# Kernel tuning notes

Hardware: AMD Instinct MI355X
Metric: run time of the kernel (lower is better)

The kernel has to match this reference:

```python
import jax, jax.numpy as jnp
import numpy as np
from jax import lax

T, B, S = 64, 64, 64
H, E, V, L = 1024, 1024, 50000, 2
PAD = 0


def setup_inputs() -> dict:
    key = jax.random.key(0)
    ks = jax.random.split(key, 12)
    sc_e = 1.0 / np.sqrt(E)
    sc_h = 1.0 / np.sqrt(H)
    inp = {
        "input": jax.random.randint(ks[0], (T, B), 0, V),
        "h0": jax.random.normal(ks[1], (L, B, H), jnp.float32),
        "c0": jax.random.normal(ks[2], (L, B, H), jnp.float32),
        "context": jax.random.normal(ks[3], (S, B, H), jnp.float32),
        # embedding table, padding row zeroed (padding_idx)
        "emb": (jax.random.normal(ks[4], (V, E), jnp.float32) * sc_e).at[PAD].set(0.0),
        # stacked LSTM params, torch gate order i,f,g,o (E == H so layers stack)
        "w_ih": jax.random.uniform(ks[5], (L, 4 * H, H), jnp.float32, -sc_h, sc_h),
        "w_hh": jax.random.uniform(ks[6], (L, 4 * H, H), jnp.float32, -sc_h, sc_h),
        "b_ih": jax.random.uniform(ks[7], (L, 4 * H), jnp.float32, -sc_h, sc_h),
        "b_hh": jax.random.uniform(ks[8], (L, 4 * H), jnp.float32, -sc_h, sc_h),
        # GlobalAttention: linear_in (H->H, no bias), linear_out (2H->H, no bias)
        "w_in": jax.random.uniform(ks[9], (H, H), jnp.float32, -sc_h, sc_h),
        "w_out": jax.random.uniform(ks[10], (H, 2 * H), jnp.float32, -sc_h, sc_h),
    }
    return inp


def _decode(input, h0, c0, context, emb, w_ih, w_hh, b_ih, b_hh, w_in, w_out):
    ctx = jnp.transpose(context, (1, 0, 2))  # [B, S, H] (context.t())
    x = emb[input]                           # [T, B, E]
    n_layers = w_ih.shape[0]

    def step(carry, x_t):
        h, c = carry  # each [L, B, H]
        layer_in = x_t
        hs, cs = [], []
        for l in range(n_layers):
            gates = layer_in @ w_ih[l].T + h[l] @ w_hh[l].T + b_ih[l] + b_hh[l]
            i, f, g, o = jnp.split(gates, 4, axis=-1)
            c_l = jax.nn.sigmoid(f) * c[l] + jax.nn.sigmoid(i) * jnp.tanh(g)
            h_l = jax.nn.sigmoid(o) * jnp.tanh(c_l)
            hs.append(h_l)
            cs.append(c_l)
            layer_in = h_l
        h_new, c_new = jnp.stack(hs), jnp.stack(cs)
        # GlobalAttention (Luong general)
        q = layer_in @ w_in.T                          # [B, H]
        scores = jnp.einsum("bsh,bh->bs", ctx, q)       # [B, S]
        a = jax.nn.softmax(scores, axis=-1)
        wc = jnp.einsum("bs,bsh->bh", a, ctx)           # [B, H]
        out = jnp.tanh(jnp.concatenate([wc, layer_in], axis=-1) @ w_out.T)
        return (h_new, c_new), (out, a)

    (h_f, c_f), (outs, attns) = lax.scan(step, (h0, c0), x)
    return outs, h_f, c_f, attns[-1]


def reference(input, h0, c0, context, emb, w_ih, w_hh, b_ih, b_hh, w_in, w_out):
    return _decode(input, h0, c0, context, emb, w_ih, w_hh, b_ih, b_hh, w_in, w_out)
```

## Files before the change

kernel.cpp:

```cpp
#include <hip/hip_runtime.h>

typedef _Float16 f16;
typedef __attribute__((ext_vector_type(4))) _Float16 f16x4;
typedef __attribute__((ext_vector_type(8))) _Float16 f16x8;
typedef __attribute__((ext_vector_type(4))) float f32x4;

__device__ __forceinline__ float fast_sig(float x) { return 1.f / (1.f + __expf(-x)); }
__device__ __forceinline__ float fast_tanh(float x) {
  float e = __expf(2.f * x);
  return 1.f - 2.f / (e + 1.f);
}

__global__ __launch_bounds__(256) void f2h_kernel(const float* __restrict__ src,
                                                  f16* __restrict__ dst) {
  size_t i = ((size_t)blockIdx.x * 256 + threadIdx.x) * 4;
  float4 v = *(const float4*)(src + i);
  dst[i + 0] = (f16)v.x;
  dst[i + 1] = (f16)v.y;
  dst[i + 2] = (f16)v.z;
  dst[i + 3] = (f16)v.w;
}

__global__ __launch_bounds__(256) void gather_rows(const float* __restrict__ emb,
                                                   const int* __restrict__ ids,
                                                   f16* __restrict__ xg) {
  int m = blockIdx.x;
  int i = threadIdx.x * 4;
  const float* src = emb + (size_t)ids[m] * 1024 + i;
  float4 v = *(const float4*)src;
  f16* d = xg + (size_t)m * 1024 + i;
  d[0] = (f16)v.x; d[1] = (f16)v.y; d[2] = (f16)v.z; d[3] = (f16)v.w;
}

__global__ __launch_bounds__(256) void init_h(const float* __restrict__ h0,
                                              f16* __restrict__ h1slot0,
                                              f16* __restrict__ h2slot0,
                                              unsigned* __restrict__ flags) {
  int i = blockIdx.x * 256 + threadIdx.x;
  h1slot0[i] = (f16)h0[i];
  h2slot0[i] = (f16)h0[65536 + i];
  if (i < 8192) flags[i] = 0;
}

__global__ __launch_bounds__(512, 1) void lstm_persistent(
    const float* __restrict__ w_ih, const float* __restrict__ w_hh,
    const float* __restrict__ b_ih, const float* __restrict__ b_hh,
    const float* __restrict__ c0,
    const f16* __restrict__ xg,
    f16* __restrict__ h1hist,
    f16* __restrict__ h2hist,
    float* __restrict__ hf, float* __restrict__ cf,
    unsigned* __restrict__ flags) {
  __shared__ f16 wlds[65536];
  __shared__ float red1[2048], red2[2048];
  __shared__ float bsum[32];
  const int p = blockIdx.x;
  const int tid = threadIdx.x;
  const int lane = tid & 63, w = tid >> 6;
  const int mt = w & 3, kh = w >> 2;
  const int am = mt * 16 + (lane & 15);
  const int kq = (lane >> 4) * 8;

  for (int s = tid; s < 8192; s += 512) {
    const int mat = s >> 11, sl = s & 2047;
    const int ln = sl & 63, ks = sl >> 6;
    const int n = ln & 15;
    const int row = (n >> 2) * 1024 + p * 4 + (n & 3) + ((mat >= 2) ? 4096 : 0);
    const int k = ks * 32 + (ln >> 4) * 8;
    const float* src = ((mat & 1) ? w_hh : w_ih) + (size_t)row * 1024 + k;
    float4 v0 = *(const float4*)src;
    float4 v1 = *(const float4*)(src + 4);
    f16x8 hv = {(f16)v0.x, (f16)v0.y, (f16)v0.z, (f16)v0.w,
                (f16)v1.x, (f16)v1.y, (f16)v1.z, (f16)v1.w};
    *(f16x8*)(wlds + (size_t)mat * 16384 + (size_t)sl * 8) = hv;
  }
  if (tid < 32) {
    int l = tid >> 4, n = tid & 15;
    int row = l * 4096 + (n >> 2) * 1024 + p * 4 + (n & 3);
    bsum[tid] = b_ih[row] + b_hh[row];
  }
  float creg;
  {
    int q = tid & 255;
    size_t idx = (size_t)(q >> 2) * 1024 + p * 4 + (q & 3);
    creg = (tid < 256) ? c0[idx] : c0[65536 + idx];
  }
  __syncthreads();

  for (int t = 0; t <= 64; ++t) {
    const int tx = (t < 64) ? t : 63;
    const int t2 = (t > 0) ? t - 1 : 0;
    const f16* xrow  = xg + ((size_t)tx * 64 + am) * 1024 + kh * 512 + kq;
    const f16* hrow  = h1hist + ((size_t)t * 64 + am) * 1024 + kh * 512 + kq;
    const f16* h2row = h2hist + ((size_t)t2 * 64 + am) * 1024 + kh * 512 + kq;

    f32x4 acc1 = {0.f, 0.f, 0.f, 0.f};
    f32x4 acc2 = {0.f, 0.f, 0.f, 0.f};
#pragma unroll
    for (int i = 0; i < 16; ++i) {
      const int ks = kh * 16 + i;
      f16x8 xv  = *(const f16x8*)(xrow + i * 32);
      f16x8 hv  = *(const f16x8*)(hrow + i * 32);
      f16x8 h2v = *(const f16x8*)(h2row + i * 32);
      f16x8 b0 = *(const f16x8*)(wlds + (size_t)ks * 512 + lane * 8);
      f16x8 b1 = *(const f16x8*)(wlds + 16384 + (size_t)ks * 512 + lane * 8);
      f16x8 b2 = *(const f16x8*)(wlds + 32768 + (size_t)ks * 512 + lane * 8);
      f16x8 b3 = *(const f16x8*)(wlds + 49152 + (size_t)ks * 512 + lane * 8);
      if (t < 64) {
        acc1 = __builtin_amdgcn_mfma_f32_16x16x32_f16(xv, b0, acc1, 0, 0, 0);
        acc1 = __builtin_amdgcn_mfma_f32_16x16x32_f16(hv, b1, acc1, 0, 0, 0);
      }
      if (t > 0) {
        acc2 = __builtin_amdgcn_mfma_f32_16x16x32_f16(hv, b2, acc2, 0, 0, 0);
        acc2 = __builtin_amdgcn_mfma_f32_16x16x32_f16(h2v, b3, acc2, 0, 0, 0);
      }
    }

    if (t < 64) {
#pragma unroll
      for (int q = 0; q < 4; q++)
        red1[w * 256 + ((lane >> 4) * 4 + q) * 16 + (lane & 15)] = acc1[q];
    }
    if (t > 0) {
#pragma unroll
      for (int q = 0; q < 4; q++)
        red2[w * 256 + ((lane >> 4) * 4 + q) * 16 + (lane & 15)] = acc2[q];
    }
    __syncthreads();

    if (t < 64 && tid < 256) {
      const int b = tid >> 2, ul = tid & 3;
      const int mrow = (b & 15) * 16, mtb = (b >> 4) * 256;
      float g4[4];
#pragma unroll
      for (int g = 0; g < 4; g++) {
        int n = g * 4 + ul;
        g4[g] = red1[mtb + mrow + n] + red1[1024 + mtb + mrow + n] + bsum[n];
      }
      float cn = fast_sig(g4[1]) * creg + fast_sig(g4[0]) * fast_tanh(g4[2]);
      float hn = fast_sig(g4[3]) * fast_tanh(cn);
      creg = cn;
      const int u = p * 4 + ul;
      if (t == 63) {
        hf[(size_t)b * 1024 + u] = hn;
        cf[(size_t)b * 1024 + u] = cn;
      }
      float h1v = __shfl_down(hn, 1, 64);
      float h2s = __shfl_down(hn, 2, 64);
      float h3v = __shfl_down(hn, 3, 64);
      if (ul == 0) {
        union { f16x4 h; unsigned long long u64; } pk;
        pk.h = (f16x4){(f16)hn, (f16)h1v, (f16)h2s, (f16)h3v};
        f16* dst = h1hist + (size_t)(t + 1) * 65536 + (size_t)b * 1024 + p * 4;
        __hip_atomic_store((unsigned long long*)dst, pk.u64,
                           __ATOMIC_RELAXED, __HIP_MEMORY_SCOPE_AGENT);
      }
    }
    if (t > 0 && tid >= 256) {
      const int q = tid & 255;
      const int b = q >> 2, ul = q & 3;
      const int mrow = (b & 15) * 16, mtb = (b >> 4) * 256;
      float g4[4];
#pragma unroll
      for (int g = 0; g < 4; g++) {
        int n = g * 4 + ul;
        g4[g] = red2[mtb + mrow + n] + red2[1024 + mtb + mrow + n] + bsum[16 + n];
      }
      float cn = fast_sig(g4[1]) * creg + fast_sig(g4[0]) * fast_tanh(g4[2]);
      float hn = fast_sig(g4[3]) * fast_tanh(cn);
      creg = cn;
      const int u = p * 4 + ul;
      if (t == 64) {
        hf[65536 + (size_t)b * 1024 + u] = hn;
        cf[65536 + (size_t)b * 1024 + u] = cn;
      }
      float h1v = __shfl_down(hn, 1, 64);
      float h2s = __shfl_down(hn, 2, 64);
      float h3v = __shfl_down(hn, 3, 64);
      if (ul == 0) {
        union { f16x4 h; unsigned long long u64; } pk;
        pk.h = (f16x4){(f16)hn, (f16)h1v, (f16)h2s, (f16)h3v};
        f16* dst = h2hist + (size_t)t * 65536 + (size_t)b * 1024 + p * 4;
        __hip_atomic_store((unsigned long long*)dst, pk.u64,
                           __ATOMIC_RELAXED, __HIP_MEMORY_SCOPE_AGENT);
      }
    }

    if (t < 64) {
      __syncthreads();
      const unsigned epoch = (unsigned)(t + 1);
      if (w == 0) {
        if (lane == 0)
          __hip_atomic_store(flags + (size_t)p * 16, epoch,
                             __ATOMIC_RELAXED, __HIP_MEMORY_SCOPE_AGENT);
        if (p == 0) {
          for (;;) {
            bool ok = true;
#pragma unroll
            for (int j = 0; j < 4; j++) {
              unsigned v = __hip_atomic_load(flags + (size_t)(lane * 4 + j) * 16,
                                             __ATOMIC_RELAXED, __HIP_MEMORY_SCOPE_AGENT);
              ok &= (v >= epoch);
            }
            if (__all(ok)) break;
            __builtin_amdgcn_s_sleep(1);
          }
          if (lane < 8)
            __hip_atomic_store(flags + 4096 + (size_t)lane * 16, epoch,
                               __ATOMIC_RELAXED, __HIP_MEMORY_SCOPE_AGENT);
        } else {
          const unsigned* go = flags + 4096 + (size_t)(p & 7) * 16;
          for (;;) {
            unsigned v = __hip_atomic_load(go, __ATOMIC_RELAXED,
                                           __HIP_MEMORY_SCOPE_AGENT);
            if (__all(v >= epoch)) break;
            __builtin_amdgcn_s_sleep(1);
          }
        }
      }
      __syncthreads();
    }
  }
}

template <typename OutT>
__global__ __launch_bounds__(256) void gemm_simple(
    const f16* __restrict__ A1, const f16* __restrict__ A2,
    const f16* __restrict__ Bm,
    const float* __restrict__ bias1, const float* __restrict__ bias2,
    OutT* __restrict__ C, int ldc,
    int K1, int Ktot, int do_tanh) {
  const int tid = threadIdx.x;
  const int lane = tid & 63;
  const int w = tid >> 6;
  const int m0 = blockIdx.y * 64 + w * 16;
  const int n0 = blockIdx.x * 64;
  const int am = m0 + (lane & 15);
  const int kq = (lane >> 4) * 8;
  const int K2 = Ktot - K1;

  f32x4 acc[4];
#pragma unroll
  for (int j = 0; j < 4; j++) acc[j] = (f32x4){0.f, 0.f, 0.f, 0.f};

  for (int k0 = 0; k0 < Ktot; k0 += 32) {
    int k = k0 + kq;
    f16x8 av;
    if (k < K1)
      av = *(const f16x8*)(A1 + (size_t)am * K1 + k);
    else
      av = *(const f16x8*)(A2 + (size_t)am * K2 + (k - K1));
#pragma unroll
    for (int j = 0; j < 4; j++) {
      f16x8 bv = *(const f16x8*)(Bm + (size_t)(n0 + j * 16 + (lane & 15)) * Ktot + k);
      acc[j] = __builtin_amdgcn_mfma_f32_16x16x32_f16(av, bv, acc[j], 0, 0, 0);
    }
  }

  const int r0 = (lane >> 4) * 4;
  const int cc = lane & 15;
#pragma unroll
  for (int j = 0; j < 4; j++) {
    int col = n0 + j * 16 + cc;
    float bv = 0.f;
    if (bias1) bv += bias1[col];
    if (bias2) bv += bias2[col];
#pragma unroll
    for (int q = 0; q < 4; q++) {
      float v = acc[j][q] + bv;
      if (do_tanh) v = fast_tanh(v);
      C[(size_t)(m0 + r0 + q) * ldc + col] = (OutT)v;
    }
  }
}

__global__ __launch_bounds__(256) void attn_kernel(
    const float* __restrict__ Q,
    const float* __restrict__ ctx,
    f16* __restrict__ wc,
    float* __restrict__ attn_out) {
  const int m = blockIdx.x;
  const int b = m & 63;
  const int t = m >> 6;
  const int tid = threadIdx.x;
  const int lane = tid & 63;
  const int w = tid >> 6;
  __shared__ float s_sc[64];
  __shared__ float s_at[64];

  const float* qp = Q + (size_t)m * 1024 + lane * 16;
  float qf[16];
#pragma unroll
  for (int i = 0; i < 4; i++) {
    float4 v = *(const float4*)(qp + i * 4);
    qf[i * 4 + 0] = v.x; qf[i * 4 + 1] = v.y; qf[i * 4 + 2] = v.z; qf[i * 4 + 3] = v.w;
  }

  for (int si = 0; si < 16; si++) {
    int s = w * 16 + si;
    const float* cp = ctx + ((size_t)s * 64 + b) * 1024 + lane * 16;
    float d = 0.f;
#pragma unroll
    for (int i = 0; i < 4; i++) {
      float4 v = *(const float4*)(cp + i * 4);
      d += v.x * qf[i * 4] + v.y * qf[i * 4 + 1] + v.z * qf[i * 4 + 2] + v.w * qf[i * 4 + 3];
    }
#pragma unroll
    for (int off = 32; off > 0; off >>= 1) d += __shfl_down(d, off, 64);
    if (lane == 0) s_sc[s] = d;
  }
  __syncthreads();
  if (w == 0) {
    float v = s_sc[lane];
    float mx = v;
#pragma unroll
    for (int off = 32; off > 0; off >>= 1) mx = fmaxf(mx, __shfl_xor(mx, off, 64));
    float e = __expf(v - mx);
    float sm = e;
#pragma unroll
    for (int off = 32; off > 0; off >>= 1) sm += __shfl_xor(sm, off, 64);
    float a = e / sm;
    s_at[lane] = a;
    if (t == 63) attn_out[b * 64 + lane] = a;
  }
  __syncthreads();
#pragma unroll
  for (int rep = 0; rep < 4; rep++) {
    int h = rep * 256 + tid;
    float acc = 0.f;
    for (int s = 0; s < 64; s++)
      acc += s_at[s] * ctx[((size_t)s * 64 + b) * 1024 + h];
    wc[(size_t)m * 1024 + h] = (f16)acc;
  }
}

extern "C" void kernel_launch(void* const* d_in, const int* in_sizes, int n_in,
                              void* d_out, int out_size, void* d_ws, size_t ws_size,
                              hipStream_t stream) {
  const int*   input = (const int*)d_in[0];
  const float* h0    = (const float*)d_in[1];
  const float* c0    = (const float*)d_in[2];
  const float* ctx   = (const float*)d_in[3];
  const float* emb   = (const float*)d_in[4];
  const float* w_ih  = (const float*)d_in[5];
  const float* w_hh  = (const float*)d_in[6];
  const float* b_ih  = (const float*)d_in[7];
  const float* b_hh  = (const float*)d_in[8];
  const float* w_in  = (const float*)d_in[9];
  const float* w_out = (const float*)d_in[10];
  float* out = (float*)d_out;

  char* ws = (char*)d_ws;
  size_t off = 0;
  auto alloc = [&](size_t bytes) {
    char* p = ws + off;
    off += (bytes + 255) & ~(size_t)255;
    return p;
  };
  f16*   h2hist = (f16*)alloc((size_t)65 * 65536 * 2);
  f16*   h1hist = (f16*)alloc((size_t)65 * 65536 * 2);
  float* Q      = (float*)alloc((size_t)4096 * 1024 * 4);
  f16*   wc     = (f16*)alloc((size_t)4096 * 1024 * 2);
  f16*   xg     = (f16*)alloc((size_t)4096 * 1024 * 2);
  f16*   winh   = (f16*)alloc((size_t)1024 * 1024 * 2);
  f16*   wouth  = (f16*)alloc((size_t)1024 * 2048 * 2);
  unsigned* flags = (unsigned*)alloc(32768);

  float* outs = out;
  float* hf   = out + (size_t)4096 * 1024;
  float* cf   = hf + 131072;
  float* attn = cf + 131072;

  f2h_kernel<<<1024, 256, 0, stream>>>(w_in, winh);
  f2h_kernel<<<2048, 256, 0, stream>>>(w_out, wouth);
  gather_rows<<<4096, 256, 0, stream>>>(emb, input, xg);
  init_h<<<256, 256, 0, stream>>>(h0, h1hist, h2hist, flags);

  {
    void* args[] = {(void*)&w_ih, (void*)&w_hh, (void*)&b_ih, (void*)&b_hh,
                    (void*)&c0, (void*)&xg, (void*)&h1hist, (void*)&h2hist,
                    (void*)&hf, (void*)&cf, (void*)&flags};
    hipLaunchCooperativeKernel(lstm_persistent, dim3(256), dim3(512), args, 0, stream);
  }

  gemm_simple<float><<<dim3(16, 64), 256, 0, stream>>>(h2hist + 65536, nullptr,
      winh, nullptr, nullptr, Q, 1024, 1024, 1024, 0);

  attn_kernel<<<4096, 256, 0, stream>>>(Q, ctx, wc, attn);

  gemm_simple<float><<<dim3(16, 64), 256, 0, stream>>>(wc, h2hist + 65536,
      wouth, nullptr, nullptr, outs, 1024, 1024, 2048, 1);
}
```

Baseline: 1.541 ms.

## Overlap input projection with grid barrier wait and stage GEMM B tiles in LDS

The persistent LSTM loop now issues the x·W_ih MFMAs for the next step before waiting on the grid-wide barrier. The flag arrival store moves to the end of each step, so the input-projection work, which needs no recurrent state, hides barrier latency. Separately, the post-LSTM GEMMs stage 64x64 B tiles in shared memory with register prefetch instead of having each wave read B directly from global memory. This adds a barrier-ordering change that must still protect the h history reads, plus extra syncthreads in the GEMM.

```diff
diff --git a/kernel.cpp b/kernel.cpp
--- a/kernel.cpp
+++ b/kernel.cpp
@@ -96,103 +96,20 @@
 
     f32x4 acc1 = {0.f, 0.f, 0.f, 0.f};
     f32x4 acc2 = {0.f, 0.f, 0.f, 0.f};
-#pragma unroll
-    for (int i = 0; i < 16; ++i) {
-      const int ks = kh * 16 + i;
-      f16x8 xv  = *(const f16x8*)(xrow + i * 32);
-      f16x8 hv  = *(const f16x8*)(hrow + i * 32);
-      f16x8 h2v = *(const f16x8*)(h2row + i * 32);
-      f16x8 b0 = *(const f16x8*)(wlds + (size_t)ks * 512 + lane * 8);
-      f16x8 b1 = *(const f16x8*)(wlds + 16384 + (size_t)ks * 512 + lane * 8);
-      f16x8 b2 = *(const f16x8*)(wlds + 32768 + (size_t)ks * 512 + lane * 8);
-      f16x8 b3 = *(const f16x8*)(wlds + 49152 + (size_t)ks * 512 + lane * 8);
-      if (t < 64) {
+
+    if (t < 64) {
+#pragma unroll
+      for (int i = 0; i < 16; ++i) {
+        const int ks = kh * 16 + i;
+        f16x8 xv = *(const f16x8*)(xrow + i * 32);
+        f16x8 b0 = *(const f16x8*)(wlds + (size_t)ks * 512 + lane * 8);
         acc1 = __builtin_amdgcn_mfma_f32_16x16x32_f16(xv, b0, acc1, 0, 0, 0);
-        acc1 = __builtin_amdgcn_mfma_f32_16x16x32_f16(hv, b1, acc1, 0, 0, 0);
-      }
-      if (t > 0) {
-        acc2 = __builtin_amdgcn_mfma_f32_16x16x32_f16(hv, b2, acc2, 0, 0, 0);
-        acc2 = __builtin_amdgcn_mfma_f32_16x16x32_f16(h2v, b3, acc2, 0, 0, 0);
-      }
-    }
-
-    if (t < 64) {
-#pragma unroll
-      for (int q = 0; q < 4; q++)
-        red1[w * 256 + ((lane >> 4) * 4 + q) * 16 + (lane & 15)] = acc1[q];
-    }
+      }
+    }
+
     if (t > 0) {
-#pragma unroll
-      for (int q = 0; q < 4; q++)
-        red2[w * 256 + ((lane >> 4) * 4 + q) * 16 + (lane & 15)] = acc2[q];
-    }
-    __syncthreads();
-
-    if (t < 64 && tid < 256) {
-      const int b = tid >> 2, ul = tid & 3;
-      const int mrow = (b & 15) * 16, mtb = (b >> 4) * 256;
-      float g4[4];
-#pragma unroll
-      for (int g = 0; g < 4; g++) {
-        int n = g * 4 + ul;
-        g4[g] = red1[mtb + mrow + n] + red1[1024 + mtb + mrow + n] + bsum[n];
-      }
-      float cn = fast_sig(g4[1]) * creg + fast_sig(g4[0]) * fast_tanh(g4[2]);
-      float hn = fast_sig(g4[3]) * fast_tanh(cn);
-      creg = cn;
-      const int u = p * 4 + ul;
-      if (t == 63) {
-        hf[(size_t)b * 1024 + u] = hn;
-        cf[(size_t)b * 1024 + u] = cn;
-      }
-      float h1v = __shfl_down(hn, 1, 64);
-      float h2s = __shfl_down(hn, 2, 64);
-      float h3v = __shfl_down(hn, 3, 64);
-      if (ul == 0) {
-        union { f16x4 h; unsigned long long u64; } pk;
-        pk.h = (f16x4){(f16)hn, (f16)h1v, (f16)h2s, (f16)h3v};
-        f16* dst = h1hist + (size_t)(t + 1) * 65536 + (size_t)b * 1024 + p * 4;
-        __hip_atomic_store((unsigned long long*)dst, pk.u64,
-                           __ATOMIC_RELAXED, __HIP_MEMORY_SCOPE_AGENT);
-      }
-    }
-    if (t > 0 && tid >= 256) {
-      const int q = tid & 255;
-      const int b = q >> 2, ul = q & 3;
-      const int mrow = (b & 15) * 16, mtb = (b >> 4) * 256;
-      float g4[4];
-#pragma unroll
-      for (int g = 0; g < 4; g++) {
-        int n = g * 4 + ul;
-        g4[g] = red2[mtb + mrow + n] + red2[1024 + mtb + mrow + n] + bsum[16 + n];
-      }
-      float cn = fast_sig(g4[1]) * creg + fast_sig(g4[0]) * fast_tanh(g4[2]);
-      float hn = fast_sig(g4[3]) * fast_tanh(cn);
-      creg = cn;
-      const int u = p * 4 + ul;
-      if (t == 64) {
-        hf[65536 + (size_t)b * 1024 + u] = hn;
-        cf[65536 + (size_t)b * 1024 + u] = cn;
-      }
-      float h1v = __shfl_down(hn, 1, 64);
-      float h2s = __shfl_down(hn, 2, 64);
-      float h3v = __shfl_down(hn, 3, 64);
-      if (ul == 0) {
-        union { f16x4 h; unsigned long long u64; } pk;
-        pk.h = (f16x4){(f16)hn, (f16)h1v, (f16)h2s, (f16)h3v};
-        f16* dst = h2hist + (size_t)t * 65536 + (size_t)b * 1024 + p * 4;
-        __hip_atomic_store((unsigned long long*)dst, pk.u64,
-                           __ATOMIC_RELAXED, __HIP_MEMORY_SCOPE_AGENT);
-      }
-    }
-
-    if (t < 64) {
-      __syncthreads();
-      const unsigned epoch = (unsigned)(t + 1);
+      const unsigned epoch = (unsigned)t;
       if (w == 0) {
-        if (lane == 0)
-          __hip_atomic_store(flags + (size_t)p * 16, epoch,
-                             __ATOMIC_RELAXED, __HIP_MEMORY_SCOPE_AGENT);
         if (p == 0) {
           for (;;) {
             bool ok = true;
@@ -220,16 +137,110 @@
       }
       __syncthreads();
     }
+
+#pragma unroll
+    for (int i = 0; i < 16; ++i) {
+      const int ks = kh * 16 + i;
+      f16x8 hv  = *(const f16x8*)(hrow + i * 32);
+      f16x8 h2v = *(const f16x8*)(h2row + i * 32);
+      f16x8 b1 = *(const f16x8*)(wlds + 16384 + (size_t)ks * 512 + lane * 8);
+      f16x8 b2 = *(const f16x8*)(wlds + 32768 + (size_t)ks * 512 + lane * 8);
+      f16x8 b3 = *(const f16x8*)(wlds + 49152 + (size_t)ks * 512 + lane * 8);
+      if (t < 64)
+        acc1 = __builtin_amdgcn_mfma_f32_16x16x32_f16(hv, b1, acc1, 0, 0, 0);
+      if (t > 0) {
+        acc2 = __builtin_amdgcn_mfma_f32_16x16x32_f16(hv, b2, acc2, 0, 0, 0);
+        acc2 = __builtin_amdgcn_mfma_f32_16x16x32_f16(h2v, b3, acc2, 0, 0, 0);
+      }
+    }
+
+    if (t < 64) {
+#pragma unroll
+      for (int q = 0; q < 4; q++)
+        red1[w * 256 + ((lane >> 4) * 4 + q) * 16 + (lane & 15)] = acc1[q];
+    }
+    if (t > 0) {
+#pragma unroll
+      for (int q = 0; q < 4; q++)
+        red2[w * 256 + ((lane >> 4) * 4 + q) * 16 + (lane & 15)] = acc2[q];
+    }
+    __syncthreads();
+
+    if (t < 64 && tid < 256) {
+      const int b = tid >> 2, ul = tid & 3;
+      const int mrow = (b & 15) * 16, mtb = (b >> 4) * 256;
+      float g4[4];
+#pragma unroll
+      for (int g = 0; g < 4; g++) {
+        int n = g * 4 + ul;
+        g4[g] = red1[mtb + mrow + n] + red1[1024 + mtb + mrow + n] + bsum[n];
+      }
+      float cn = fast_sig(g4[1]) * creg + fast_sig(g4[0]) * fast_tanh(g4[2]);
+      float hn = fast_sig(g4[3]) * fast_tanh(cn);
+      creg = cn;
+      const int u = p * 4 + ul;
+      if (t == 63) {
+        hf[(size_t)b * 1024 + u] = hn;
+        cf[(size_t)b * 1024 + u] = cn;
+      }
+      float h1v = __shfl_down(hn, 1, 64);
+      float h2s = __shfl_down(hn, 2, 64);
+      float h3v = __shfl_down(hn, 3, 64);
+      if (ul == 0) {
+        union { f16x4 h; unsigned long long u64; } pk;
+        pk.h = (f16x4){(f16)hn, (f16)h1v, (f16)h2s, (f16)h3v};
+        f16* dst = h1hist + (size_t)(t + 1) * 65536 + (size_t)b * 1024 + p * 4;
+        __hip_atomic_store((unsigned long long*)dst, pk.u64,
+                           __ATOMIC_RELAXED, __HIP_MEMORY_SCOPE_AGENT);
+      }
+    }
+    if (t > 0 && tid >= 256) {
+      const int q = tid & 255;
+      const int b = q >> 2, ul = q & 3;
+      const int mrow = (b & 15) * 16, mtb = (b >> 4) * 256;
+      float g4[4];
+#pragma unroll
+      for (int g = 0; g < 4; g++) {
+        int n = g * 4 + ul;
+        g4[g] = red2[mtb + mrow + n] + red2[1024 + mtb + mrow + n] + bsum[16 + n];
+      }
+      float cn = fast_sig(g4[1]) * creg + fast_sig(g4[0]) * fast_tanh(g4[2]);
+      float hn = fast_sig(g4[3]) * fast_tanh(cn);
+      creg = cn;
+      const int u = p * 4 + ul;
+      if (t == 64) {
+        hf[65536 + (size_t)b * 1024 + u] = hn;
+        cf[65536 + (size_t)b * 1024 + u] = cn;
+      }
+      float h1v = __shfl_down(hn, 1, 64);
+      float h2s = __shfl_down(hn, 2, 64);
+      float h3v = __shfl_down(hn, 3, 64);
+      if (ul == 0) {
+        union { f16x4 h; unsigned long long u64; } pk;
+        pk.h = (f16x4){(f16)hn, (f16)h1v, (f16)h2s, (f16)h3v};
+        f16* dst = h2hist + (size_t)t * 65536 + (size_t)b * 1024 + p * 4;
+        __hip_atomic_store((unsigned long long*)dst, pk.u64,
+                           __ATOMIC_RELAXED, __HIP_MEMORY_SCOPE_AGENT);
+      }
+    }
+
+    if (t < 64) {
+      __syncthreads();
+      if (w == 0 && lane == 0)
+        __hip_atomic_store(flags + (size_t)p * 16, (unsigned)(t + 1),
+                           __ATOMIC_RELAXED, __HIP_MEMORY_SCOPE_AGENT);
+    }
   }
 }
 
 template <typename OutT>
-__global__ __launch_bounds__(256) void gemm_simple(
+__global__ __launch_bounds__(256) void gemm_lds(
     const f16* __restrict__ A1, const f16* __restrict__ A2,
     const f16* __restrict__ Bm,
     const float* __restrict__ bias1, const float* __restrict__ bias2,
     OutT* __restrict__ C, int ldc,
     int K1, int Ktot, int do_tanh) {
+  __shared__ f16 bt[64][72];
   const int tid = threadIdx.x;
   const int lane = tid & 63;
   const int w = tid >> 6;
@@ -238,22 +249,39 @@
   const int am = m0 + (lane & 15);
   const int kq = (lane >> 4) * 8;
   const int K2 = Ktot - K1;
+  const int br = tid >> 2;
+  const int bs = (tid & 3) * 16;
 
   f32x4 acc[4];
 #pragma unroll
   for (int j = 0; j < 4; j++) acc[j] = (f32x4){0.f, 0.f, 0.f, 0.f};
 
-  for (int k0 = 0; k0 < Ktot; k0 += 32) {
-    int k = k0 + kq;
-    f16x8 av;
-    if (k < K1)
-      av = *(const f16x8*)(A1 + (size_t)am * K1 + k);
-    else
-      av = *(const f16x8*)(A2 + (size_t)am * K2 + (k - K1));
-#pragma unroll
-    for (int j = 0; j < 4; j++) {
-      f16x8 bv = *(const f16x8*)(Bm + (size_t)(n0 + j * 16 + (lane & 15)) * Ktot + k);
-      acc[j] = __builtin_amdgcn_mfma_f32_16x16x32_f16(av, bv, acc[j], 0, 0, 0);
+  const f16* bsrc = Bm + (size_t)(n0 + br) * Ktot + bs;
+  f16x8 s0 = *(const f16x8*)(bsrc);
+  f16x8 s1 = *(const f16x8*)(bsrc + 8);
+
+  for (int kc = 0; kc < Ktot; kc += 64) {
+    __syncthreads();
+    *(f16x8*)&bt[br][bs] = s0;
+    *(f16x8*)&bt[br][bs + 8] = s1;
+    __syncthreads();
+    if (kc + 64 < Ktot) {
+      s0 = *(const f16x8*)(bsrc + kc + 64);
+      s1 = *(const f16x8*)(bsrc + kc + 64 + 8);
+    }
+#pragma unroll
+    for (int kk = 0; kk < 64; kk += 32) {
+      int k = kc + kk + kq;
+      f16x8 av;
+      if (k < K1)
+        av = *(const f16x8*)(A1 + (size_t)am * K1 + k);
+      else
+        av = *(const f16x8*)(A2 + (size_t)am * K2 + (k - K1));
+#pragma unroll
+      for (int j = 0; j < 4; j++) {
+        f16x8 bv = *(const f16x8*)&bt[j * 16 + (lane & 15)][kk + kq];
+        acc[j] = __builtin_amdgcn_mfma_f32_16x16x32_f16(av, bv, acc[j], 0, 0, 0);
+      }
     }
   }
 
@@ -383,11 +411,11 @@
     hipLaunchCooperativeKernel(lstm_persistent, dim3(256), dim3(512), args, 0, stream);
   }
 
-  gemm_simple<float><<<dim3(16, 64), 256, 0, stream>>>(h2hist + 65536, nullptr,
+  gemm_lds<float><<<dim3(16, 64), 256, 0, stream>>>(h2hist + 65536, nullptr,
       winh, nullptr, nullptr, Q, 1024, 1024, 1024, 0);
 
   attn_kernel<<<4096, 256, 0, stream>>>(Q, ctx, wc, attn);
 
-  gemm_simple<float><<<dim3(16, 64), 256, 0, stream>>>(wc, h2hist + 65536,
+  gemm_lds<float><<<dim3(16, 64), 256, 0, stream>>>(wc, h2hist + 65536,
       wouth, nullptr, nullptr, outs, 1024, 1024, 2048, 1);
 }
```

Result: faster. 1.327 ms (-13.9%).
